# Performance work log

Measured on AMD Instinct MI355X. Metric: run time of the kernel, lower is better.

Reference implementation:

```python
import jax, jax.numpy as jnp
import numpy as np

INPUT_SIZE = 1024
HIDDEN_SIZE = 1024
BATCH = 8192


def setup_inputs() -> dict:
    key = jax.random.key(0)
    ks = jax.random.split(key, 14)
    stdv = 1.0 / HIDDEN_SIZE ** 0.5
    u = lambda k, shape: jax.random.uniform(k, shape, jnp.float32, -stdv, stdv)
    H, I = HIDDEN_SIZE, INPUT_SIZE
    return {
        "x": jax.random.normal(ks[0], (BATCH, I), jnp.float32),
        "hidden": jax.random.normal(ks[1], (BATCH, H), jnp.float32),
        "weight_xr": u(ks[2], (H, I)),
        "weight_hr": u(ks[3], (H, H)),
        "bias_r": u(ks[4], (H,)),
        "weight_xz": u(ks[5], (H, I)),
        "weight_hz": u(ks[6], (H, H)),
        "bias_z": u(ks[7], (H,)),
        "weight_xh": u(ks[8], (H, I)),
        "weight_hh": u(ks[9], (H, H)),
        "bias_h": u(ks[10], (H,)),
        "weight_c": u(ks[11], (H, I + H)),
        "bias_c": u(ks[12], (H,)),
        "weight_hat_h": u(ks[13], (H, I + H)),
        "bias_hat_h": u(jax.random.fold_in(key, 99), (H,)),
    }


def reference(x, hidden, weight_xr, weight_hr, bias_r, weight_xz, weight_hz, bias_z,
              weight_xh, weight_hh, bias_h, weight_c, bias_c, weight_hat_h, bias_hat_h):
    # combined: [B, I+H]
    combined = jnp.concatenate([x, hidden], axis=1)
    c_t = combined @ weight_c.T + bias_c                      # [B, H]
    a_t = jax.nn.softmax(c_t, axis=1)
    hat_h_t = a_t * jax.nn.relu(combined @ weight_hat_h.T + bias_hat_h)
    r_t = jax.nn.sigmoid(x @ weight_xr.T + bias_r + hidden @ weight_hr.T)
    z_t = jax.nn.sigmoid(x @ weight_xz.T + bias_z + hidden @ weight_hz.T)
    h_tilde = jnp.tanh(x @ weight_xh.T + bias_h + (r_t * hidden) @ weight_hh.T)
    h_t = (1.0 - z_t) * h_tilde + z_t * hidden + hat_h_t
    return h_t
```

## Files before the change

kernel.cpp:

```cpp
#include <hip/hip_runtime.h>

typedef unsigned short ushort_t;
typedef __attribute__((ext_vector_type(8))) short short8;
typedef __attribute__((ext_vector_type(4))) float float4v;
typedef __attribute__((ext_vector_type(4))) ushort_t ushort4v;

#define B_ROWS 8192
#define HDIM   1024
#define GLD    5120

__device__ __forceinline__ float bf2f(ushort_t u) {
    return __uint_as_float(((unsigned)u) << 16);
}
__device__ __forceinline__ ushort_t f2bf(float f) {
    unsigned u = __float_as_uint(f);
    u += 0x7FFFu + ((u >> 16) & 1u);
    return (ushort_t)(u >> 16);
}

__global__ __launch_bounds__(256) void pack_all(
    const float* __restrict__ x, const float* __restrict__ h,
    const float* __restrict__ wc, const float* __restrict__ what,
    const float* __restrict__ wxr, const float* __restrict__ whr,
    const float* __restrict__ wxz, const float* __restrict__ whz,
    const float* __restrict__ wxh, const float* __restrict__ whh,
    ushort_t* __restrict__ A, ushort_t* __restrict__ W,
    ushort_t* __restrict__ Whh)
{
    const int bid = blockIdx.x;
    float4v v;
    ushort_t* dst;
    size_t i4;
    if (bid < 16384) {
        i4 = ((size_t)bid * 256 + threadIdx.x) * 4;
        int c = (int)(i4 & 2047);
        size_t b = i4 >> 11;
        const float* src = (c < 1024) ? (x + b * 1024 + c)
                                      : (h + b * 1024 + (c - 1024));
        v = *(const float4v*)src;
        dst = A + i4;
    } else if (bid < 26624) {
        i4 = ((size_t)(bid - 16384) * 256 + threadIdx.x) * 4;
        int j = (int)(i4 >> 11);
        int k = (int)(i4 & 2047);
        int r = j >> 10, jr = j & 1023;
        if (r == 0) {
            v = *(const float4v*)(wc + (size_t)j * 2048 + k);
        } else if (r == 1) {
            v = *(const float4v*)(what + (size_t)jr * 2048 + k);
        } else if (r == 4) {
            v = (k < 1024) ? *(const float4v*)(wxh + (size_t)jr * 1024 + k)
                           : (float4v){0.f, 0.f, 0.f, 0.f};
        } else {
            const float* p0 = (r == 2) ? wxr : wxz;
            const float* p1 = (r == 2) ? whr : whz;
            const float* p = (k < 1024) ? (p0 + (size_t)jr * 1024 + k)
                                        : (p1 + (size_t)jr * 1024 + (k - 1024));
            v = *(const float4v*)p;
        }
        dst = W + i4;
    } else {
        i4 = ((size_t)(bid - 26624) * 256 + threadIdx.x) * 4;
        v = *(const float4v*)(whh + i4);
        dst = Whh + i4;
    }
    ushort4v o;
#pragma unroll
    for (int t = 0; t < 4; ++t) o[t] = f2bf(v[t]);
    *(ushort4v*)dst = o;
}

__global__ __launch_bounds__(256) void gemm1(
    const ushort_t* __restrict__ A, const ushort_t* __restrict__ B,
    ushort_t* __restrict__ C)
{
    const int bn0 = blockIdx.x * 128;
    const int bm0 = blockIdx.y * 128;
    const int K = (bn0 >= 4096) ? 1024 : 2048;

    __shared__ ushort_t As[128 * 32];
    __shared__ ushort_t Bs[128 * 32];

    const int t = threadIdx.x;
    const int wave = t >> 6, lane = t & 63;
    const int wr = wave >> 1, wcq = wave & 1;
    const int q = lane >> 4, r16 = lane & 15;
    const int lrow = lane >> 2;
    const int lcol = (lane & 3) * 8;

    float4v acc[4][4];
#pragma unroll
    for (int i = 0; i < 4; ++i)
#pragma unroll
        for (int j = 0; j < 4; ++j)
            acc[i][j] = {0.f, 0.f, 0.f, 0.f};

    for (int k0 = 0; k0 < K; k0 += 32) {
        if (wave < 2) {
#pragma unroll
            for (int j = 0; j < 4; ++j) {
                int c = wave * 4 + j;
                const ushort_t* gp = A + (size_t)(bm0 + c * 16 + lrow) * 2048 + k0 + lcol;
                __builtin_amdgcn_global_load_lds(
                    (const __attribute__((address_space(1))) void*)gp,
                    (__attribute__((address_space(3))) void*)(As + c * 512),
                    16, 0, 0);
            }
        } else {
#pragma unroll
            for (int j = 0; j < 4; ++j) {
                int c = (wave - 2) * 4 + j;
                const ushort_t* gp = B + (size_t)(bn0 + c * 16 + lrow) * 2048 + k0 + lcol;
                __builtin_amdgcn_global_load_lds(
                    (const __attribute__((address_space(1))) void*)gp,
                    (__attribute__((address_space(3))) void*)(Bs + c * 512),
                    16, 0, 0);
            }
        }
        __syncthreads();

        short8 af[4], bf[4];
#pragma unroll
        for (int mi = 0; mi < 4; ++mi)
            af[mi] = *(const short8*)&As[(wr * 64 + mi * 16 + r16) * 32 + q * 8];
#pragma unroll
        for (int ni = 0; ni < 4; ++ni)
            bf[ni] = *(const short8*)&Bs[(wcq * 64 + ni * 16 + r16) * 32 + q * 8];
#pragma unroll
        for (int mi = 0; mi < 4; ++mi)
#pragma unroll
            for (int ni = 0; ni < 4; ++ni)
                acc[mi][ni] = __builtin_amdgcn_mfma_f32_16x16x32_bf16(
                    af[mi], bf[ni], acc[mi][ni], 0, 0, 0);
        __syncthreads();
    }

#pragma unroll
    for (int mi = 0; mi < 4; ++mi)
#pragma unroll
        for (int ni = 0; ni < 4; ++ni)
#pragma unroll
            for (int reg = 0; reg < 4; ++reg) {
                int row = bm0 + wr * 64 + mi * 16 + q * 4 + reg;
                int col = bn0 + wcq * 64 + ni * 16 + r16;
                C[(size_t)row * GLD + col] = f2bf(acc[mi][ni][reg]);
            }
}

__global__ __launch_bounds__(256) void row_pass(
    ushort_t* __restrict__ G, const float* __restrict__ bias_c,
    const float* __restrict__ bias_hat, const float* __restrict__ bias_r,
    const float* __restrict__ hidden, ushort_t* __restrict__ rh)
{
    const int wave = threadIdx.x >> 6, lane = threadIdx.x & 63;
    const size_t row = (size_t)blockIdx.x * 4 + wave;
    ushort_t* g = G + row * GLD;
    const int c0 = lane * 16;

    float cv[16];
    {
        short8 a = *(const short8*)(g + c0);
        short8 b = *(const short8*)(g + c0 + 8);
#pragma unroll
        for (int i = 0; i < 8; ++i) {
            cv[i]     = bf2f((ushort_t)a[i]) + bias_c[c0 + i];
            cv[8 + i] = bf2f((ushort_t)b[i]) + bias_c[c0 + 8 + i];
        }
    }
    float mx = cv[0];
#pragma unroll
    for (int i = 1; i < 16; ++i) mx = fmaxf(mx, cv[i]);
#pragma unroll
    for (int m = 1; m < 64; m <<= 1) mx = fmaxf(mx, __shfl_xor(mx, m));
    float sum = 0.f;
#pragma unroll
    for (int i = 0; i < 16; ++i) { cv[i] = __expf(cv[i] - mx); sum += cv[i]; }
#pragma unroll
    for (int m = 1; m < 64; m <<= 1) sum += __shfl_xor(sum, m);
    const float inv = 1.0f / sum;

    {
        short8 a = *(const short8*)(g + 1024 + c0);
        short8 b = *(const short8*)(g + 1024 + c0 + 8);
        short8 oa, ob;
#pragma unroll
        for (int i = 0; i < 8; ++i) {
            float ha = bf2f((ushort_t)a[i]) + bias_hat[c0 + i];
            float hb = bf2f((ushort_t)b[i]) + bias_hat[c0 + 8 + i];
            oa[i] = (short)f2bf(cv[i] * inv * fmaxf(ha, 0.f));
            ob[i] = (short)f2bf(cv[8 + i] * inv * fmaxf(hb, 0.f));
        }
        *(short8*)(g + c0) = oa;
        *(short8*)(g + c0 + 8) = ob;
    }

    {
        short8 a = *(const short8*)(g + 2048 + c0);
        short8 b = *(const short8*)(g + 2048 + c0 + 8);
        const float* hp = hidden + row * 1024 + c0;
        short8 oa, ob;
#pragma unroll
        for (int i = 0; i < 8; ++i) {
            float ra = 1.0f / (1.0f + __expf(-(bf2f((ushort_t)a[i]) + bias_r[c0 + i])));
            float rb = 1.0f / (1.0f + __expf(-(bf2f((ushort_t)b[i]) + bias_r[c0 + 8 + i])));
            oa[i] = (short)f2bf(ra * hp[i]);
            ob[i] = (short)f2bf(rb * hp[8 + i]);
        }
        ushort_t* rp = rh + row * 1024 + c0;
        *(short8*)rp = oa;
        *(short8*)(rp + 8) = ob;
    }
}

__global__ __launch_bounds__(256) void gemm2_final(
    const ushort_t* __restrict__ A, const ushort_t* __restrict__ B,
    const ushort_t* __restrict__ G, const float* __restrict__ bias_z,
    const float* __restrict__ bias_h, const float* __restrict__ hidden,
    float* __restrict__ out)
{
    const int bn0 = blockIdx.x * 128;
    const int bm0 = blockIdx.y * 128;

    __shared__ ushort_t As[128 * 32];
    __shared__ ushort_t Bs[128 * 32];

    const int t = threadIdx.x;
    const int wave = t >> 6, lane = t & 63;
    const int wr = wave >> 1, wcq = wave & 1;
    const int q = lane >> 4, r16 = lane & 15;
    const int lrow = lane >> 2;
    const int lcol = (lane & 3) * 8;

    float4v acc[4][4];
#pragma unroll
    for (int i = 0; i < 4; ++i)
#pragma unroll
        for (int j = 0; j < 4; ++j)
            acc[i][j] = {0.f, 0.f, 0.f, 0.f};

    for (int k0 = 0; k0 < 1024; k0 += 32) {
        if (wave < 2) {
#pragma unroll
            for (int j = 0; j < 4; ++j) {
                int c = wave * 4 + j;
                const ushort_t* gp = A + (size_t)(bm0 + c * 16 + lrow) * 1024 + k0 + lcol;
                __builtin_amdgcn_global_load_lds(
                    (const __attribute__((address_space(1))) void*)gp,
                    (__attribute__((address_space(3))) void*)(As + c * 512),
                    16, 0, 0);
            }
        } else {
#pragma unroll
            for (int j = 0; j < 4; ++j) {
                int c = (wave - 2) * 4 + j;
                const ushort_t* gp = B + (size_t)(bn0 + c * 16 + lrow) * 1024 + k0 + lcol;
                __builtin_amdgcn_global_load_lds(
                    (const __attribute__((address_space(1))) void*)gp,
                    (__attribute__((address_space(3))) void*)(Bs + c * 512),
                    16, 0, 0);
            }
        }
        __syncthreads();

        short8 af[4], bf[4];
#pragma unroll
        for (int mi = 0; mi < 4; ++mi)
            af[mi] = *(const short8*)&As[(wr * 64 + mi * 16 + r16) * 32 + q * 8];
#pragma unroll
        for (int ni = 0; ni < 4; ++ni)
            bf[ni] = *(const short8*)&Bs[(wcq * 64 + ni * 16 + r16) * 32 + q * 8];
#pragma unroll
        for (int mi = 0; mi < 4; ++mi)
#pragma unroll
            for (int ni = 0; ni < 4; ++ni)
                acc[mi][ni] = __builtin_amdgcn_mfma_f32_16x16x32_bf16(
                    af[mi], bf[ni], acc[mi][ni], 0, 0, 0);
        __syncthreads();
    }

#pragma unroll
    for (int mi = 0; mi < 4; ++mi)
#pragma unroll
        for (int ni = 0; ni < 4; ++ni) {
            const int col = bn0 + wcq * 64 + ni * 16 + r16;
            const float bz = bias_z[col];
            const float bh = bias_h[col];
#pragma unroll
            for (int reg = 0; reg < 4; ++reg) {
                const int row = bm0 + wr * 64 + mi * 16 + q * 4 + reg;
                const ushort_t* grow = G + (size_t)row * GLD;
                float z = 1.0f / (1.0f + __expf(-(bf2f(grow[3072 + col]) + bz)));
                float targ = bf2f(grow[4096 + col]) + bh + acc[mi][ni][reg];
                float th = 1.0f - 2.0f / (__expf(2.0f * targ) + 1.0f);
                out[(size_t)row * 1024 + col] =
                    (1.0f - z) * th + z * hidden[(size_t)row * 1024 + col]
                    + bf2f(grow[col]);
            }
        }
}


extern "C" void kernel_launch(void* const* d_in, const int* in_sizes, int n_in,
                              void* d_out, int out_size, void* d_ws, size_t ws_size,
                              hipStream_t stream)
{
    const float* x        = (const float*)d_in[0];
    const float* hidden   = (const float*)d_in[1];
    const float* wxr      = (const float*)d_in[2];
    const float* whr      = (const float*)d_in[3];
    const float* bias_r   = (const float*)d_in[4];
    const float* wxz      = (const float*)d_in[5];
    const float* whz      = (const float*)d_in[6];
    const float* bias_z   = (const float*)d_in[7];
    const float* wxh      = (const float*)d_in[8];
    const float* whh      = (const float*)d_in[9];
    const float* bias_h   = (const float*)d_in[10];
    const float* wc       = (const float*)d_in[11];
    const float* bias_c   = (const float*)d_in[12];
    const float* what     = (const float*)d_in[13];
    const float* bias_hat = (const float*)d_in[14];
    float* out = (float*)d_out;

    char* ws = (char*)d_ws;
    ushort_t* G     = (ushort_t*)(ws);
    ushort_t* Abf   = (ushort_t*)(ws + 83886080);
    ushort_t* Wbf   = (ushort_t*)(ws + 117440512);
    ushort_t* Whhbf = (ushort_t*)(ws + 138412032);
    ushort_t* rhbf  = (ushort_t*)(ws + 140509184);

    pack_all<<<27648, 256, 0, stream>>>(x, hidden, wc, what, wxr, whr, wxz, whz,
                                        wxh, whh, Abf, Wbf, Whhbf);

    gemm1<<<dim3(40, 64), 256, 0, stream>>>(Abf, Wbf, G);

    row_pass<<<B_ROWS / 4, 256, 0, stream>>>(G, bias_c, bias_hat, bias_r, hidden, rhbf);

    gemm2_final<<<dim3(8, 64), 256, 0, stream>>>(rhbf, Whhbf, G, bias_z, bias_h,
                                                 hidden, out);
}
```

Before: 419.5 us.

## Enlarge gemm1 tile to 256x128 and stage gemm2 epilogue through LDS

gemm1 now computes a 256x128 output tile per block, with each wave owning 64 rows by all 128 columns, so each block reuses the B tile across twice as many rows and the grid halves. All waves now share the global-to-LDS load work. The gemm2_final epilogue writes the accumulators to LDS as bf16, then reads them back row-major so the G, hidden and out accesses are coalesced across threads. Costs: more accumulator registers in gemm1, which may limit occupancy, and an extra bf16 rounding of the gemm2 accumulator before tanh.

```diff
diff --git a/kernel.cpp b/kernel.cpp
--- a/kernel.cpp
+++ b/kernel.cpp
@@ -70,66 +70,61 @@
     *(ushort4v*)dst = o;
 }
 
-__global__ __launch_bounds__(256) void gemm1(
+__global__ __launch_bounds__(256, 2) void gemm1(
     const ushort_t* __restrict__ A, const ushort_t* __restrict__ B,
     ushort_t* __restrict__ C)
 {
     const int bn0 = blockIdx.x * 128;
-    const int bm0 = blockIdx.y * 128;
+    const int bm0 = blockIdx.y * 256;
     const int K = (bn0 >= 4096) ? 1024 : 2048;
 
-    __shared__ ushort_t As[128 * 32];
+    __shared__ ushort_t As[256 * 32];
     __shared__ ushort_t Bs[128 * 32];
 
     const int t = threadIdx.x;
     const int wave = t >> 6, lane = t & 63;
-    const int wr = wave >> 1, wcq = wave & 1;
     const int q = lane >> 4, r16 = lane & 15;
     const int lrow = lane >> 2;
     const int lcol = (lane & 3) * 8;
 
-    float4v acc[4][4];
+    float4v acc[4][8];
 #pragma unroll
     for (int i = 0; i < 4; ++i)
 #pragma unroll
-        for (int j = 0; j < 4; ++j)
+        for (int j = 0; j < 8; ++j)
             acc[i][j] = {0.f, 0.f, 0.f, 0.f};
 
     for (int k0 = 0; k0 < K; k0 += 32) {
-        if (wave < 2) {
-#pragma unroll
-            for (int j = 0; j < 4; ++j) {
-                int c = wave * 4 + j;
-                const ushort_t* gp = A + (size_t)(bm0 + c * 16 + lrow) * 2048 + k0 + lcol;
+#pragma unroll
+        for (int j = 0; j < 6; ++j) {
+            int l = wave * 6 + j;
+            if (l < 16) {
+                const ushort_t* gp = A + (size_t)(bm0 + l * 16 + lrow) * 2048 + k0 + lcol;
                 __builtin_amdgcn_global_load_lds(
                     (const __attribute__((address_space(1))) void*)gp,
-                    (__attribute__((address_space(3))) void*)(As + c * 512),
+                    (__attribute__((address_space(3))) void*)(As + l * 512),
                     16, 0, 0);
-            }
-        } else {
-#pragma unroll
-            for (int j = 0; j < 4; ++j) {
-                int c = (wave - 2) * 4 + j;
-                const ushort_t* gp = B + (size_t)(bn0 + c * 16 + lrow) * 2048 + k0 + lcol;
+            } else {
+                const ushort_t* gp = B + (size_t)(bn0 + (l - 16) * 16 + lrow) * 2048 + k0 + lcol;
                 __builtin_amdgcn_global_load_lds(
                     (const __attribute__((address_space(1))) void*)gp,
-                    (__attribute__((address_space(3))) void*)(Bs + c * 512),
+                    (__attribute__((address_space(3))) void*)(Bs + (l - 16) * 512),
                     16, 0, 0);
             }
         }
         __syncthreads();
 
-        short8 af[4], bf[4];
+        short8 af[4], bf[8];
 #pragma unroll
         for (int mi = 0; mi < 4; ++mi)
-            af[mi] = *(const short8*)&As[(wr * 64 + mi * 16 + r16) * 32 + q * 8];
-#pragma unroll
-        for (int ni = 0; ni < 4; ++ni)
-            bf[ni] = *(const short8*)&Bs[(wcq * 64 + ni * 16 + r16) * 32 + q * 8];
+            af[mi] = *(const short8*)&As[(wave * 64 + mi * 16 + r16) * 32 + q * 8];
+#pragma unroll
+        for (int ni = 0; ni < 8; ++ni)
+            bf[ni] = *(const short8*)&Bs[(ni * 16 + r16) * 32 + q * 8];
 #pragma unroll
         for (int mi = 0; mi < 4; ++mi)
 #pragma unroll
-            for (int ni = 0; ni < 4; ++ni)
+            for (int ni = 0; ni < 8; ++ni)
                 acc[mi][ni] = __builtin_amdgcn_mfma_f32_16x16x32_bf16(
                     af[mi], bf[ni], acc[mi][ni], 0, 0, 0);
         __syncthreads();
@@ -138,11 +133,11 @@
 #pragma unroll
     for (int mi = 0; mi < 4; ++mi)
 #pragma unroll
-        for (int ni = 0; ni < 4; ++ni)
+        for (int ni = 0; ni < 8; ++ni)
 #pragma unroll
             for (int reg = 0; reg < 4; ++reg) {
-                int row = bm0 + wr * 64 + mi * 16 + q * 4 + reg;
-                int col = bn0 + wcq * 64 + ni * 16 + r16;
+                int row = bm0 + wave * 64 + mi * 16 + q * 4 + reg;
+                int col = bn0 + ni * 16 + r16;
                 C[(size_t)row * GLD + col] = f2bf(acc[mi][ni][reg]);
             }
 }
@@ -212,6 +207,7 @@
     }
 }
 
+#define CSTRIDE 132
 __global__ __launch_bounds__(256) void gemm2_final(
     const ushort_t* __restrict__ A, const ushort_t* __restrict__ B,
     const ushort_t* __restrict__ G, const float* __restrict__ bias_z,
@@ -221,8 +217,9 @@
     const int bn0 = blockIdx.x * 128;
     const int bm0 = blockIdx.y * 128;
 
-    __shared__ ushort_t As[128 * 32];
-    __shared__ ushort_t Bs[128 * 32];
+    __shared__ ushort_t smem[128 * CSTRIDE];
+    ushort_t* As = smem;
+    ushort_t* Bs = smem + 4096;
 
     const int t = threadIdx.x;
     const int wave = t >> 6, lane = t & 63;
@@ -281,22 +278,31 @@
 #pragma unroll
     for (int mi = 0; mi < 4; ++mi)
 #pragma unroll
-        for (int ni = 0; ni < 4; ++ni) {
-            const int col = bn0 + wcq * 64 + ni * 16 + r16;
-            const float bz = bias_z[col];
-            const float bh = bias_h[col];
+        for (int ni = 0; ni < 4; ++ni)
 #pragma unroll
             for (int reg = 0; reg < 4; ++reg) {
-                const int row = bm0 + wr * 64 + mi * 16 + q * 4 + reg;
-                const ushort_t* grow = G + (size_t)row * GLD;
-                float z = 1.0f / (1.0f + __expf(-(bf2f(grow[3072 + col]) + bz)));
-                float targ = bf2f(grow[4096 + col]) + bh + acc[mi][ni][reg];
-                float th = 1.0f - 2.0f / (__expf(2.0f * targ) + 1.0f);
-                out[(size_t)row * 1024 + col] =
-                    (1.0f - z) * th + z * hidden[(size_t)row * 1024 + col]
-                    + bf2f(grow[col]);
-            }
-        }
+                int rl = wr * 64 + mi * 16 + q * 4 + reg;
+                int cl = wcq * 64 + ni * 16 + r16;
+                smem[rl * CSTRIDE + cl] = f2bf(acc[mi][ni][reg]);
+            }
+    __syncthreads();
+
+    const int colL = t & 127;
+    const int gc = bn0 + colL;
+    const float bz = bias_z[gc];
+    const float bh = bias_h[gc];
+    const int rbase = t >> 7;
+#pragma unroll 4
+    for (int pass = 0; pass < 64; ++pass) {
+        const int rowL = pass * 2 + rbase;
+        const size_t gr = (size_t)(bm0 + rowL);
+        const ushort_t* grow = G + gr * GLD;
+        float z = 1.0f / (1.0f + __expf(-(bf2f(grow[3072 + gc]) + bz)));
+        float targ = bf2f(grow[4096 + gc]) + bh + bf2f(smem[rowL * CSTRIDE + colL]);
+        float th = 1.0f - 2.0f / (__expf(2.0f * targ) + 1.0f);
+        out[gr * 1024 + gc] =
+            (1.0f - z) * th + z * hidden[gr * 1024 + gc] + bf2f(grow[gc]);
+    }
 }
 
 
@@ -331,7 +337,7 @@
     pack_all<<<27648, 256, 0, stream>>>(x, hidden, wc, what, wxr, whr, wxz, whz,
                                         wxh, whh, Abf, Wbf, Whhbf);
 
-    gemm1<<<dim3(40, 64), 256, 0, stream>>>(Abf, Wbf, G);
+    gemm1<<<dim3(40, 32), 256, 0, stream>>>(Abf, Wbf, G);
 
     row_pass<<<B_ROWS / 4, 256, 0, stream>>>(G, bias_c, bias_hat, bias_r, hidden, rhbf);
 
```

Result: no change. 427.3 us (+1.8%).
